# Kernel tuning notes

Measured on AMD Instinct MI355X. Metric: run time of the kernel, lower is better.

Reference implementation:

```python
import jax, jax.numpy as jnp
import numpy as np

# Model / problem constants (from init_kwargs and chosen shapes)
N = 2048          # num_neurons
T = 4096          # number of Euler steps / save points
MAX_SPIKES = 256  # event buffer size
V_RESET = 1.0
ALPHA = 0.01
T0, T1 = 0.0, 1.0


def intensity_fn(v):
    return jax.nn.softplus(v)


def setup_inputs() -> dict:
    key = jax.random.key(0)
    ks = jax.random.split(key, 7)
    # learned weights: uniform in [0.5, 1.0) as in _build_w (network mask all-False)
    w = jax.random.uniform(ks[0], (N, N), minval=0.5, maxval=1.0)
    mu = jax.random.uniform(ks[1], (2,), minval=0.5, maxval=1.0)
    v0 = jax.random.uniform(ks[2], (N,))
    i0 = jax.random.uniform(ks[3], (N,))
    ic = jax.random.uniform(ks[4], (T, N)) * 0.5          # input current per step
    u_init = jax.random.uniform(ks[5], (N,), minval=1e-6, maxval=1.0)
    u_resample = jax.random.uniform(ks[6], (T, N), minval=1e-6, maxval=1.0)
    return dict(w=w, mu=mu, v0=v0, i0=i0, ic=ic, u_init=u_init, u_resample=u_resample)


def reference(w, mu, v0, i0, ic, u_init, u_resample):
    dt = (T1 - T0) / T
    mu1, mu2 = mu[0], mu[1]
    # initial state: s0 = log(U) - alpha  (spike clock), y = [v, i, s] per neuron
    s0 = jnp.log(u_init) - ALPHA
    y0 = jnp.stack([v0, i0, s0], axis=-1)  # [N, 3]

    tevents0 = jnp.full((MAX_SPIKES,), jnp.inf, dtype=jnp.float32)
    yevents0 = jnp.full((MAX_SPIKES, N, 3), jnp.inf, dtype=jnp.float32)
    etypes0 = jnp.zeros((MAX_SPIKES, N), dtype=bool)

    def step(carry, xs):
        y, cnt, tev, yev, et = carry
        t_idx, ic_t, u_t = xs
        v, i, s = y[:, 0], y[:, 1], y[:, 2]
        # drift_vf: v' = mu1*(i + ic - v); i' = -mu2*i; s' = intensity(v)
        v1 = v + dt * (mu1 * (i + ic_t - v))
        i1 = i + dt * (-mu2 * i)
        s1 = s + dt * intensity_fn(v)
        mask = s1 >= 0.0                 # per-neuron event mask (cond_fn: y[n,2] crossing 0)
        event = jnp.any(mask)
        write = event & (cnt < MAX_SPIKES)
        idx = jnp.minimum(cnt, MAX_SPIKES - 1)
        tnow = T0 + (t_idx + 1.0) * dt
        yevent = jnp.stack([v1, i1, s1], axis=-1)  # [N, 3]
        # dynamic scatter writes into event buffers keyed by spike counter
        tev = tev.at[idx].set(jnp.where(write, tnow, tev[idx]))
        yev = yev.at[idx].set(jnp.where(write, yevent, yev[idx]))
        et = et.at[idx].set(jnp.where(write, mask, et[idx]))
        # transition fn: reset v, inject w row of first spiking neuron, resample s
        event_idx = jnp.argmax(mask)
        w_row = jnp.where(event, w[event_idx], jnp.zeros((N,), w.dtype))
        v2 = v1 - jnp.where(mask, V_RESET, 0.0)
        i2 = i1 + w_row
        s2 = jnp.where(mask, jnp.log(u_t) - ALPHA, s1)
        ytrans = jnp.stack([v2, i2, s2], axis=-1)
        y_new = jnp.where(event, ytrans, yevent)
        cnt = cnt + jnp.where(write, 1, 0)
        return (y_new, cnt, tev, yev, et), y_new

    xs = (jnp.arange(T, dtype=jnp.float32), ic, u_resample)
    carry0 = (y0, jnp.int32(0), tevents0, yevents0, etypes0)
    (yT, num_spikes, tevents, yevents, event_types), ys = jax.lax.scan(step, carry0, xs)
    return ys, tevents, yevents, event_types, num_spikes
```

## Files before the change

kernel.cpp:

```cpp
#include <hip/hip_runtime.h>
#include <cmath>
#include <climits>

#define N_ 2048
#define T_ 4096
#define MAXSP 256
#define CHUNK 256
#define NCHUNK (T_ / CHUNK)

#define WS_EIDX_OFF   0
#define WS_CNT_OFF    (T_ * 4)
#define WS_SNAP_OFF   (T_ * 4 + NCHUNK * 4)

typedef float f2 __attribute__((ext_vector_type(2)));

__device__ __forceinline__ int imin(int a, int b) { return a < b ? a : b; }

__device__ __forceinline__ void lds_barrier() {
    asm volatile("s_waitcnt lgkmcnt(0)\n\ts_barrier" ::: "memory");
}

__global__ void snn_init_tail(float* __restrict__ out) {
    const size_t base    = (size_t)T_ * N_ * 3;
    const size_t inf_cnt = (size_t)MAXSP + (size_t)MAXSP * N_ * 3;
    const size_t tot     = inf_cnt + (size_t)MAXSP * N_;
    size_t idx = (size_t)blockIdx.x * blockDim.x + threadIdx.x;
    if (idx < tot) {
        out[base + idx] = (idx < inf_cnt) ? __builtin_inff() : 0.0f;
    }
}

extern "C" __global__ void __launch_bounds__(1024)
snn_scan(const float* __restrict__ w,   const float* __restrict__ mu,
         const float* __restrict__ v0,  const float* __restrict__ i0,
         const float* __restrict__ ic,  const float* __restrict__ u_init,
         const float* __restrict__ u_re, float* __restrict__ out,
         int* __restrict__ ws_eidx, int* __restrict__ ws_cnt,
         float* __restrict__ ws_snap)
{
#pragma clang fp contract(off)
    const int tid = threadIdx.x;
    const int n0  = tid * 2;
    const int wv  = tid >> 6, lane = tid & 63;
    const float dt = 1.0f / 4096.0f;
    const float mu1 = mu[0], mu2 = mu[1];

    float* tev = out + (size_t)T_ * N_ * 3;
    float* nsp = tev + MAXSP + (size_t)MAXSP * N_ * 3 + (size_t)MAXSP * N_;

    f2 vc, sc, i1p;
    vc  = *(const f2*)(v0 + n0);
    i1p = *(const f2*)(i0 + n0);
    { f2 a = *(const f2*)(u_init + n0);
      sc.x = logf(a.x) - 0.01f; sc.y = logf(a.y) - 0.01f; }

    bool evp = false;
    f2 w2; w2.x = 0.0f; w2.y = 0.0f;

    __shared__ int red[4];
    if (tid == 0) { red[0] = INT_MAX; red[1] = INT_MAX;
                    red[2] = INT_MAX; red[3] = INT_MAX; }

    const float* icp = ic + n0;
    const float* up  = u_re + n0;
    f2 icA = *(const f2*)(icp);
    f2 icB = *(const f2*)(icp + N_);
    f2 uA  = *(const f2*)(up);
    f2 uB  = *(const f2*)(up + N_);
    icp += 2 * N_; up += 2 * N_;

    lds_barrier();

    int cnt = 0;
#pragma unroll 4
    for (int k = 0; k < T_; ++k) {
        f2 sp;
        bool slow = (fminf(vc.x, vc.y) < 16.0f);
        if (__ballot(slow)) {
            sp.x = fmaxf(vc.x, 0.0f) + __logf(1.0f + __expf(-fabsf(vc.x)));
            sp.y = fmaxf(vc.y, 0.0f) + __logf(1.0f + __expf(-fabsf(vc.y)));
        } else {
            sp = vc;
        }
        f2 s1 = sc + dt * sp;
        bool m0 = (s1.x >= 0.0f), m1 = (s1.y >= 0.0f);

        unsigned long long b0 = __ballot(m0);
        unsigned long long b1 = __ballot(b1 == b1 ? m1 : m1);
        b1 = __ballot(m1);
        if (b0 | b1) {
            int c0 = b0 ? (((int)__ffsll((long long)b0) - 1) << 1)
                        : INT_MAX;
            int c1 = b1 ? ((((int)__ffsll((long long)b1) - 1) << 1) | 1)
                        : INT_MAX;
            int cand = (wv << 7) + imin(c0, c1);
            if (lane == 0) atomicMin(&red[k & 3], cand);
        }

        lds_barrier();
        int eidx = red[k & 3];
        eidx = __builtin_amdgcn_readfirstlane(eidx);
        if (tid == 0) red[(k + 2) & 3] = INT_MAX;

        f2 ip = i1p;
        if (evp) ip += w2;

        if ((k & (CHUNK - 1)) == 0) {
            const int c = k >> 8;
            float* spn = ws_snap + (size_t)c * 3 * N_;
            *(f2*)(spn + n0)          = vc;
            *(f2*)(spn + N_ + n0)     = ip;
            *(f2*)(spn + 2 * N_ + n0) = sc;
            if (tid == 0) ws_cnt[c] = cnt;
        }

        f2 v1 = vc + dt * (mu1 * ((ip + icA) - vc));
        i1p   = ip + dt * ((-mu2) * ip);

        evp = (eidx != INT_MAX);
        vc.x = m0 ? (v1.x - 1.0f) : v1.x;
        vc.y = m1 ? (v1.y - 1.0f) : v1.y;
        if (evp) {
            w2 = *(const f2*)(w + (size_t)eidx * N_ + n0);
            sc.x = m0 ? (__logf(uA.x) - 0.01f) : s1.x;
            sc.y = m1 ? (__logf(uA.y) - 0.01f) : s1.y;
            if (tid == 0) {
                ws_eidx[k] = eidx;
                if (cnt < MAXSP) tev[cnt] = (float)(k + 1) * dt;
            }
            if (cnt < MAXSP) cnt++;
        } else {
            sc = s1;
            if (tid == 0) ws_eidx[k] = -1;
        }

        icA = icB; uA = uB;
        if (k + 2 < T_) {
            icB = *(const f2*)icp;
            uB  = *(const f2*)up;
            icp += N_; up += N_;
        }
    }

    if (tid == 0) nsp[0] = (float)cnt;
}

extern "C" __global__ void __launch_bounds__(256)
snn_replay(const float* __restrict__ w,   const float* __restrict__ mu,
           const float* __restrict__ ic,  const float* __restrict__ u_re,
           float* __restrict__ out,
           const int* __restrict__ ws_eidx, const int* __restrict__ ws_cnt,
           const float* __restrict__ ws_snap)
{
#pragma clang fp contract(off)
    const int c = blockIdx.x >> 3;
    const int n = ((blockIdx.x & 7) << 8) + threadIdx.x;
    const float dt = 1.0f / 4096.0f;
    const float mu1 = mu[0], mu2 = mu[1];

    float* ys  = out;
    float* yev = out + (size_t)T_ * N_ * 3 + MAXSP;
    float* et  = yev + (size_t)MAXSP * N_ * 3;

    const float* sp = ws_snap + (size_t)c * 3 * N_;
    float v  = sp[n];
    float ii = sp[N_ + n];
    float ss = sp[2 * N_ + n];
    int cnt = ws_cnt[c];

    const int t0 = c << 8;
    const float* icp = ic + (size_t)t0 * N_ + n;
    const float* up  = u_re + (size_t)t0 * N_ + n;
    float* yr = ys + ((size_t)t0 * N_ + n) * 3;

    for (int k = 0; k < CHUNK; ++k) {
        const int t = t0 + k;
        const int e = ws_eidx[t];
        const float icv = icp[0];

        float v1 = v + dt * (mu1 * ((ii + icv) - v));
        float i1 = ii + dt * ((-mu2) * ii);
        float spv;
        if (__ballot(v < 16.0f)) {
            spv = fmaxf(v, 0.0f) + __logf(1.0f + __expf(-fabsf(v)));
        } else {
            spv = v;
        }
        float s1 = ss + dt * spv;
        bool m = (s1 >= 0.0f);

        if (e >= 0) {
            float wv_ = w[(size_t)e * N_ + n];
            float uu  = up[0];
            if (cnt < MAXSP) {
                float* ye = yev + ((size_t)cnt * N_ + n) * 3;
                ye[0] = v1; ye[1] = i1; ye[2] = s1;
                et[(size_t)cnt * N_ + n] = m ? 1.0f : 0.0f;
                cnt++;
            }
            v  = m ? (v1 - 1.0f) : v1;
            ii = i1 + wv_;
            ss = m ? (__logf(uu) - 0.01f) : s1;
        } else {
            v = v1; ii = i1; ss = s1;
        }

        yr[0] = v; yr[1] = ii; yr[2] = ss;

        icp += N_; up += N_; yr += (size_t)3 * N_;
    }
}

extern "C" void kernel_launch(void* const* d_in, const int* in_sizes, int n_in,
                              void* d_out, int out_size, void* d_ws, size_t ws_size,
                              hipStream_t stream) {
    const float* w      = (const float*)d_in[0];
    const float* mu     = (const float*)d_in[1];
    const float* v0     = (const float*)d_in[2];
    const float* i0     = (const float*)d_in[3];
    const float* ic     = (const float*)d_in[4];
    const float* u_init = (const float*)d_in[5];
    const float* u_re   = (const float*)d_in[6];
    float* out = (float*)d_out;

    char* ws = (char*)d_ws;
    int*   ws_eidx = (int*)(ws + WS_EIDX_OFF);
    int*   ws_cnt  = (int*)(ws + WS_CNT_OFF);
    float* ws_snap = (float*)(ws + WS_SNAP_OFF);

    const size_t tail = (size_t)MAXSP + (size_t)MAXSP * N_ * 3 + (size_t)MAXSP * N_;
    int blocks = (int)((tail + 255) / 256);
    snn_init_tail<<<blocks, 256, 0, stream>>>(out);

    snn_scan<<<1, 1024, 0, stream>>>(w, mu, v0, i0, ic, u_init, u_re,
                                     out, ws_eidx, ws_cnt, ws_snap);

    snn_replay<<<NCHUNK * 8, 256, 0, stream>>>(w, mu, ic, u_re, out,
                                               ws_eidx, ws_cnt, ws_snap);
}
```

Measured before the change: 3.099 ms.

## Software-pipeline scan step: compute next event mask before barrier, prefetch w row early

Restructures the serial scan loop so that the next step's spike-clock update, event mask and atomicMin reduction are computed before the single per-step barrier. The selected weight row is loaded right after reading the reduction result, so the global load has a full iteration to complete before it is used. The ic/u prefetch depth grows from two to three steps. The intent is to shorten the critical path per step by hiding the weight-row load latency and removing barrier-adjacent stalls, at the cost of more live registers and a more intricate reset-slot rotation for the LDS reduction.

```diff
diff --git a/kernel.cpp b/kernel.cpp
--- a/kernel.cpp
+++ b/kernel.cpp
@@ -48,14 +48,15 @@
     float* tev = out + (size_t)T_ * N_ * 3;
     float* nsp = tev + MAXSP + (size_t)MAXSP * N_ * 3 + (size_t)MAXSP * N_;
 
-    f2 vc, sc, i1p;
-    vc  = *(const f2*)(v0 + n0);
-    i1p = *(const f2*)(i0 + n0);
+    f2 vA, sA, iRaw;
+    vA   = *(const f2*)(v0 + n0);
+    iRaw = *(const f2*)(i0 + n0);
     { f2 a = *(const f2*)(u_init + n0);
-      sc.x = logf(a.x) - 0.01f; sc.y = logf(a.y) - 0.01f; }
-
-    bool evp = false;
-    f2 w2; w2.x = 0.0f; w2.y = 0.0f;
+      sA.x = logf(a.x) - 0.01f; sA.y = logf(a.y) - 0.01f; }
+
+    bool evP = false;
+    f2 w2;   w2.x = 0.0f; w2.y = 0.0f;
+    f2 wNew; wNew.x = 0.0f; wNew.y = 0.0f;
 
     __shared__ int red[4];
     if (tid == 0) { red[0] = INT_MAX; red[1] = INT_MAX;
@@ -65,79 +66,105 @@
     const float* up  = u_re + n0;
     f2 icA = *(const f2*)(icp);
     f2 icB = *(const f2*)(icp + N_);
+    f2 icC = *(const f2*)(icp + 2 * N_);
     f2 uA  = *(const f2*)(up);
     f2 uB  = *(const f2*)(up + N_);
-    icp += 2 * N_; up += 2 * N_;
-
+    f2 uC  = *(const f2*)(up + 2 * N_);
+    icp += 3 * N_; up += 3 * N_;
+
+    lds_barrier();
+
+    f2 s1c; bool m0c, m1c;
+    {
+        f2 sp;
+        bool slow = (fminf(vA.x, vA.y) < 16.0f);
+        if (__ballot(slow)) {
+            sp.x = fmaxf(vA.x, 0.0f) + __logf(1.0f + __expf(-fabsf(vA.x)));
+            sp.y = fmaxf(vA.y, 0.0f) + __logf(1.0f + __expf(-fabsf(vA.y)));
+        } else {
+            sp = vA;
+        }
+        s1c = sA + dt * sp;
+        m0c = (s1c.x >= 0.0f); m1c = (s1c.y >= 0.0f);
+        unsigned long long b0 = __ballot(m0c);
+        unsigned long long b1 = __ballot(m1c);
+        if (b0 | b1) {
+            int c0 = b0 ? (((int)__ffsll((long long)b0) - 1) << 1) : INT_MAX;
+            int c1 = b1 ? ((((int)__ffsll((long long)b1) - 1) << 1) | 1) : INT_MAX;
+            int cand = (wv << 7) + imin(c0, c1);
+            if (lane == 0) atomicMin(&red[0], cand);
+        }
+    }
     lds_barrier();
 
     int cnt = 0;
 #pragma unroll 4
     for (int k = 0; k < T_; ++k) {
-        f2 sp;
-        bool slow = (fminf(vc.x, vc.y) < 16.0f);
-        if (__ballot(slow)) {
-            sp.x = fmaxf(vc.x, 0.0f) + __logf(1.0f + __expf(-fabsf(vc.x)));
-            sp.y = fmaxf(vc.y, 0.0f) + __logf(1.0f + __expf(-fabsf(vc.y)));
-        } else {
-            sp = vc;
-        }
-        f2 s1 = sc + dt * sp;
-        bool m0 = (s1.x >= 0.0f), m1 = (s1.y >= 0.0f);
-
-        unsigned long long b0 = __ballot(m0);
-        unsigned long long b1 = __ballot(b1 == b1 ? m1 : m1);
-        b1 = __ballot(m1);
-        if (b0 | b1) {
-            int c0 = b0 ? (((int)__ffsll((long long)b0) - 1) << 1)
-                        : INT_MAX;
-            int c1 = b1 ? ((((int)__ffsll((long long)b1) - 1) << 1) | 1)
-                        : INT_MAX;
-            int cand = (wv << 7) + imin(c0, c1);
-            if (lane == 0) atomicMin(&red[k & 3], cand);
-        }
-
-        lds_barrier();
         int eidx = red[k & 3];
         eidx = __builtin_amdgcn_readfirstlane(eidx);
-        if (tid == 0) red[(k + 2) & 3] = INT_MAX;
-
-        f2 ip = i1p;
-        if (evp) ip += w2;
+        const bool evK = (eidx != INT_MAX);
+        if (evK) wNew = *(const f2*)(w + (size_t)eidx * N_ + n0);
+
+        f2 ip = iRaw;
+        if (evP) ip += w2;
 
         if ((k & (CHUNK - 1)) == 0) {
             const int c = k >> 8;
             float* spn = ws_snap + (size_t)c * 3 * N_;
-            *(f2*)(spn + n0)          = vc;
+            *(f2*)(spn + n0)          = vA;
             *(f2*)(spn + N_ + n0)     = ip;
-            *(f2*)(spn + 2 * N_ + n0) = sc;
+            *(f2*)(spn + 2 * N_ + n0) = sA;
             if (tid == 0) ws_cnt[c] = cnt;
         }
 
-        f2 v1 = vc + dt * (mu1 * ((ip + icA) - vc));
-        i1p   = ip + dt * ((-mu2) * ip);
-
-        evp = (eidx != INT_MAX);
-        vc.x = m0 ? (v1.x - 1.0f) : v1.x;
-        vc.y = m1 ? (v1.y - 1.0f) : v1.y;
-        if (evp) {
-            w2 = *(const f2*)(w + (size_t)eidx * N_ + n0);
-            sc.x = m0 ? (__logf(uA.x) - 0.01f) : s1.x;
-            sc.y = m1 ? (__logf(uA.y) - 0.01f) : s1.y;
+        f2 v1 = vA + dt * (mu1 * ((ip + icA) - vA));
+        iRaw  = ip + dt * ((-mu2) * ip);
+
+        vA.x = m0c ? (v1.x - 1.0f) : v1.x;
+        vA.y = m1c ? (v1.y - 1.0f) : v1.y;
+        if (evK) {
+            sA.x = m0c ? (__logf(uA.x) - 0.01f) : s1c.x;
+            sA.y = m1c ? (__logf(uA.y) - 0.01f) : s1c.y;
             if (tid == 0) {
                 ws_eidx[k] = eidx;
                 if (cnt < MAXSP) tev[cnt] = (float)(k + 1) * dt;
             }
             if (cnt < MAXSP) cnt++;
         } else {
-            sc = s1;
+            sA = s1c;
             if (tid == 0) ws_eidx[k] = -1;
         }
-
-        icA = icB; uA = uB;
-        if (k + 2 < T_) {
-            icB = *(const f2*)icp;
-            uB  = *(const f2*)up;
+        evP = evK;
+        w2  = wNew;
+
+        if (k + 1 < T_) {
+            f2 sp;
+            bool slow = (fminf(vA.x, vA.y) < 16.0f);
+            if (__ballot(slow)) {
+                sp.x = fmaxf(vA.x, 0.0f) + __logf(1.0f + __expf(-fabsf(vA.x)));
+                sp.y = fmaxf(vA.y, 0.0f) + __logf(1.0f + __expf(-fabsf(vA.y)));
+            } else {
+                sp = vA;
+            }
+            s1c = sA + dt * sp;
+            m0c = (s1c.x >= 0.0f); m1c = (s1c.y >= 0.0f);
+            unsigned long long b0 = __ballot(m0c);
+            unsigned long long b1 = __ballot(m1c);
+            if (b0 | b1) {
+                int c0 = b0 ? (((int)__ffsll((long long)b0) - 1) << 1) : INT_MAX;
+                int c1 = b1 ? ((((int)__ffsll((long long)b1) - 1) << 1) | 1) : INT_MAX;
+                int cand = (wv << 7) + imin(c0, c1);
+                if (lane == 0) atomicMin(&red[(k + 1) & 3], cand);
+            }
+        }
+
+        lds_barrier();
+        if (tid == 0) red[(k + 3) & 3] = INT_MAX;
+
+        icA = icB; icB = icC; uA = uB; uB = uC;
+        if (k + 3 < T_) {
+            icC = *(const f2*)icp;
+            uC  = *(const f2*)up;
             icp += N_; up += N_;
         }
     }
```

After: 3.801 ms. +22.7%, slower.

## Process two time steps per block barrier in sequential scan

Applied to the files above, without the earlier changes.

Restructures the single-block scan so each barrier covers two Euler steps. The second step's v and s updates are computed locally, using the fact that the event's w row only feeds the i state, which affects v one step later. The w-row gathers and the event bookkeeping for both steps are resolved after one shared reduction, with a wider 8-slot LDS ring. This halves the number of workgroup barriers on the serial critical path, at the cost of more live registers and more complex per-iteration code.

```diff
diff --git a/kernel.cpp b/kernel.cpp
--- a/kernel.cpp
+++ b/kernel.cpp
@@ -7,6 +7,7 @@
 #define MAXSP 256
 #define CHUNK 256
 #define NCHUNK (T_ / CHUNK)
+#define NBODY (CHUNK / 2)
 
 #define WS_EIDX_OFF   0
 #define WS_CNT_OFF    (T_ * 4)
@@ -48,97 +49,154 @@
     float* tev = out + (size_t)T_ * N_ * 3;
     float* nsp = tev + MAXSP + (size_t)MAXSP * N_ * 3 + (size_t)MAXSP * N_;
 
-    f2 vc, sc, i1p;
-    vc  = *(const f2*)(v0 + n0);
-    i1p = *(const f2*)(i0 + n0);
-    { f2 a = *(const f2*)(u_init + n0);
-      sc.x = logf(a.x) - 0.01f; sc.y = logf(a.y) - 0.01f; }
-
-    bool evp = false;
-    f2 w2; w2.x = 0.0f; w2.y = 0.0f;
-
-    __shared__ int red[4];
-    if (tid == 0) { red[0] = INT_MAX; red[1] = INT_MAX;
-                    red[2] = INT_MAX; red[3] = INT_MAX; }
+    f2 vP, sP, iP;
+    vP = *(const f2*)(v0 + n0);
+    iP = *(const f2*)(i0 + n0);
+    { f2 a_ = *(const f2*)(u_init + n0);
+      sP.x = logf(a_.x) - 0.01f; sP.y = logf(a_.y) - 0.01f; }
+
+    __shared__ __align__(16) int red[8];
+    if (tid == 0) {
+        red[0] = INT_MAX; red[1] = INT_MAX; red[2] = INT_MAX; red[3] = INT_MAX;
+        red[4] = INT_MAX; red[5] = INT_MAX; red[6] = INT_MAX; red[7] = INT_MAX;
+    }
 
     const float* icp = ic + n0;
     const float* up  = u_re + n0;
-    f2 icA = *(const f2*)(icp);
-    f2 icB = *(const f2*)(icp + N_);
-    f2 uA  = *(const f2*)(up);
-    f2 uB  = *(const f2*)(up + N_);
-    icp += 2 * N_; up += 2 * N_;
+    f2 ic0 = *(const f2*)(icp);
+    f2 ic1 = *(const f2*)(icp + N_);
+    f2 ic2 = *(const f2*)(icp + 2 * N_);
+    f2 ic3 = *(const f2*)(icp + 3 * N_);
+    f2 u0  = *(const f2*)(up);
+    f2 u1  = *(const f2*)(up + N_);
+    f2 u2  = *(const f2*)(up + 2 * N_);
+    f2 u3  = *(const f2*)(up + 3 * N_);
+    icp += 4 * N_; up += 4 * N_;
 
     lds_barrier();
 
     int cnt = 0;
-#pragma unroll 4
-    for (int k = 0; k < T_; ++k) {
-        f2 sp;
-        bool slow = (fminf(vc.x, vc.y) < 16.0f);
-        if (__ballot(slow)) {
-            sp.x = fmaxf(vc.x, 0.0f) + __logf(1.0f + __expf(-fabsf(vc.x)));
-            sp.y = fmaxf(vc.y, 0.0f) + __logf(1.0f + __expf(-fabsf(vc.y)));
-        } else {
-            sp = vc;
-        }
-        f2 s1 = sc + dt * sp;
-        bool m0 = (s1.x >= 0.0f), m1 = (s1.y >= 0.0f);
-
-        unsigned long long b0 = __ballot(m0);
-        unsigned long long b1 = __ballot(b1 == b1 ? m1 : m1);
-        b1 = __ballot(m1);
-        if (b0 | b1) {
-            int c0 = b0 ? (((int)__ffsll((long long)b0) - 1) << 1)
-                        : INT_MAX;
-            int c1 = b1 ? ((((int)__ffsll((long long)b1) - 1) << 1) | 1)
-                        : INT_MAX;
-            int cand = (wv << 7) + imin(c0, c1);
-            if (lane == 0) atomicMin(&red[k & 3], cand);
-        }
-
-        lds_barrier();
-        int eidx = red[k & 3];
-        eidx = __builtin_amdgcn_readfirstlane(eidx);
-        if (tid == 0) red[(k + 2) & 3] = INT_MAX;
-
-        f2 ip = i1p;
-        if (evp) ip += w2;
-
-        if ((k & (CHUNK - 1)) == 0) {
-            const int c = k >> 8;
+    for (int c = 0; c < NCHUNK; ++c) {
+        {
             float* spn = ws_snap + (size_t)c * 3 * N_;
-            *(f2*)(spn + n0)          = vc;
-            *(f2*)(spn + N_ + n0)     = ip;
-            *(f2*)(spn + 2 * N_ + n0) = sc;
+            *(f2*)(spn + n0)          = vP;
+            *(f2*)(spn + N_ + n0)     = iP;
+            *(f2*)(spn + 2 * N_ + n0) = sP;
             if (tid == 0) ws_cnt[c] = cnt;
         }
 
-        f2 v1 = vc + dt * (mu1 * ((ip + icA) - vc));
-        i1p   = ip + dt * ((-mu2) * ip);
-
-        evp = (eidx != INT_MAX);
-        vc.x = m0 ? (v1.x - 1.0f) : v1.x;
-        vc.y = m1 ? (v1.y - 1.0f) : v1.y;
-        if (evp) {
-            w2 = *(const f2*)(w + (size_t)eidx * N_ + n0);
-            sc.x = m0 ? (__logf(uA.x) - 0.01f) : s1.x;
-            sc.y = m1 ? (__logf(uA.y) - 0.01f) : s1.y;
+        for (int j = 0; j < NBODY; ++j) {
+            const int a  = (c << 8) + (j << 1);
+            const int bj = (c << 7) + j;
+            const int p  = (bj & 3) << 1;
+
+            f2 spA;
+            bool slowA = (fminf(vP.x, vP.y) < 16.0f);
+            if (__ballot(slowA)) {
+                spA.x = fmaxf(vP.x, 0.0f) + __logf(1.0f + __expf(-fabsf(vP.x)));
+                spA.y = fmaxf(vP.y, 0.0f) + __logf(1.0f + __expf(-fabsf(vP.y)));
+            } else {
+                spA = vP;
+            }
+            f2 s1a = sP + dt * spA;
+            bool ma0 = (s1a.x >= 0.0f), ma1 = (s1a.y >= 0.0f);
+            unsigned long long ba0 = __ballot(ma0);
+            unsigned long long ba1 = __ballot(ma1);
+            bool anyA = ((ba0 | ba1) != 0ull);
+            if (anyA) {
+                int c0 = ba0 ? (((int)__ffsll((long long)ba0) - 1) << 1)       : INT_MAX;
+                int c1 = ba1 ? ((((int)__ffsll((long long)ba1) - 1) << 1) | 1) : INT_MAX;
+                int cand = (wv << 7) + imin(c0, c1);
+                if (lane == 0) atomicMin(&red[p], cand);
+            }
+
+            f2 v1a = vP + dt * (mu1 * ((iP + ic0) - vP));
+            f2 i1a = iP + dt * ((-mu2) * iP);
+            f2 va, sa;
+            va.x = ma0 ? (v1a.x - 1.0f) : v1a.x;
+            va.y = ma1 ? (v1a.y - 1.0f) : v1a.y;
+            if (anyA) {
+                sa.x = ma0 ? (__logf(u0.x) - 0.01f) : s1a.x;
+                sa.y = ma1 ? (__logf(u0.y) - 0.01f) : s1a.y;
+            } else {
+                sa = s1a;
+            }
+
+            f2 spB;
+            bool slowB = (fminf(va.x, va.y) < 16.0f);
+            if (__ballot(slowB)) {
+                spB.x = fmaxf(va.x, 0.0f) + __logf(1.0f + __expf(-fabsf(va.x)));
+                spB.y = fmaxf(va.y, 0.0f) + __logf(1.0f + __expf(-fabsf(va.y)));
+            } else {
+                spB = va;
+            }
+            f2 s1b = sa + dt * spB;
+            bool mb0 = (s1b.x >= 0.0f), mb1 = (s1b.y >= 0.0f);
+            unsigned long long bb0 = __ballot(mb0);
+            unsigned long long bb1 = __ballot(mb1);
+            bool anyB = ((bb0 | bb1) != 0ull);
+            if (anyB) {
+                int c0 = bb0 ? (((int)__ffsll((long long)bb0) - 1) << 1)       : INT_MAX;
+                int c1 = bb1 ? ((((int)__ffsll((long long)bb1) - 1) << 1) | 1) : INT_MAX;
+                int cand = (wv << 7) + imin(c0, c1);
+                if (lane == 0) atomicMin(&red[p + 1], cand);
+            }
+
+            lds_barrier();
+            int2 rr = *(const int2*)(&red[p]);
+            int eA = __builtin_amdgcn_readfirstlane(rr.x);
+            int eB = __builtin_amdgcn_readfirstlane(rr.y);
             if (tid == 0) {
-                ws_eidx[k] = eidx;
-                if (cnt < MAXSP) tev[cnt] = (float)(k + 1) * dt;
-            }
-            if (cnt < MAXSP) cnt++;
-        } else {
-            sc = s1;
-            if (tid == 0) ws_eidx[k] = -1;
-        }
-
-        icA = icB; uA = uB;
-        if (k + 2 < T_) {
-            icB = *(const f2*)icp;
-            uB  = *(const f2*)up;
-            icp += N_; up += N_;
+                const int q = (p + 4) & 7;
+                red[q] = INT_MAX; red[q + 1] = INT_MAX;
+            }
+
+            f2 iA = i1a;
+            if (eA != INT_MAX) {
+                f2 wA = *(const f2*)(w + (size_t)eA * N_ + n0);
+                iA += wA;
+                if (tid == 0) {
+                    ws_eidx[a] = eA;
+                    if (cnt < MAXSP) tev[cnt] = (float)(a + 1) * dt;
+                }
+                if (cnt < MAXSP) cnt++;
+            } else if (tid == 0) {
+                ws_eidx[a] = -1;
+            }
+
+            f2 v1b = va + dt * (mu1 * ((iA + ic1) - va));
+            f2 i1b = iA + dt * ((-mu2) * iA);
+            vP.x = mb0 ? (v1b.x - 1.0f) : v1b.x;
+            vP.y = mb1 ? (v1b.y - 1.0f) : v1b.y;
+            if (anyB) {
+                sP.x = mb0 ? (__logf(u1.x) - 0.01f) : s1b.x;
+                sP.y = mb1 ? (__logf(u1.y) - 0.01f) : s1b.y;
+            } else {
+                sP = s1b;
+            }
+
+            f2 iB = i1b;
+            if (eB != INT_MAX) {
+                f2 wB = *(const f2*)(w + (size_t)eB * N_ + n0);
+                iB += wB;
+                if (tid == 0) {
+                    ws_eidx[a + 1] = eB;
+                    if (cnt < MAXSP) tev[cnt] = (float)(a + 2) * dt;
+                }
+                if (cnt < MAXSP) cnt++;
+            } else if (tid == 0) {
+                ws_eidx[a + 1] = -1;
+            }
+            iP = iB;
+
+            ic0 = ic2; ic1 = ic3; u0 = u2; u1 = u3;
+            if (a + 6 <= T_) {
+                ic2 = *(const f2*)(icp);
+                ic3 = *(const f2*)(icp + N_);
+                u2  = *(const f2*)(up);
+                u3  = *(const f2*)(up + N_);
+                icp += 2 * N_; up += 2 * N_;
+            }
         }
     }
 
```

Result: slower. 4.937 ms (+59.3%).
